# Kernel tuning notes

Hardware: AMD Instinct MI355X
Metric: run time of the kernel (lower is better)

Reference implementation:

```python
import jax, jax.numpy as jnp
import numpy as np

B, S, D, H = 4, 2048, 1024, 16
DEPTH = D // H  # 64


def setup_inputs() -> dict:
    key = jax.random.key(0)
    ks = jax.random.split(key, 11)
    scale = 1.0 / np.sqrt(D)
    inp = {
        "v": jax.random.normal(ks[0], (B, S, D), jnp.float32),
        "k": jax.random.normal(ks[1], (B, S, D), jnp.float32),
        "q": jax.random.normal(ks[2], (B, S, D), jnp.float32),
        # causal mask: 1.0 where attention is disallowed (strict upper triangle)
        "mask": jnp.triu(jnp.ones((S, S), jnp.float32), k=1)[None, None, :, :],
        "wq": jax.random.normal(ks[3], (D, D), jnp.float32) * scale,
        "bq": jnp.zeros((D,), jnp.float32),
        "wk": jax.random.normal(ks[4], (D, D), jnp.float32) * scale,
        "bk": jnp.zeros((D,), jnp.float32),
        "wv": jax.random.normal(ks[5], (D, D), jnp.float32) * scale,
        "bv": jnp.zeros((D,), jnp.float32),
        "wo": jax.random.normal(ks[6], (D, D), jnp.float32) * scale,
        "bo": jnp.zeros((D,), jnp.float32),
    }
    return inp


def _split_heads(x):
    # [B, S, D] -> [B, H, S, depth]
    b, s, _ = x.shape
    return x.reshape(b, s, H, DEPTH).transpose(0, 2, 1, 3)


def reference(v, k, q, mask, wq, bq, wk, bk, wv, bv, wo, bo):
    qh = _split_heads(q @ wq + bq)  # [B,H,S,depth]
    kh = _split_heads(k @ wk + bk)
    vh = _split_heads(v @ wv + bv)

    logits = jnp.einsum("bhqd,bhkd->bhqk", qh, kh) / jnp.sqrt(
        jnp.asarray(DEPTH, jnp.float32)
    )
    logits = logits + mask * -1e9
    attn = jax.nn.softmax(logits, axis=-1)  # [B,H,S,S]
    out = jnp.einsum("bhqk,bhkd->bhqd", attn, vh)
    out = out.transpose(0, 2, 1, 3).reshape(q.shape[0], -1, D)  # [B,S,D]
    return out @ wo + bo
```

## Files before the change

kernel.cpp:

```cpp
#include <hip/hip_runtime.h>

typedef _Float16 f16;
typedef _Float16 half8 __attribute__((ext_vector_type(8)));
typedef _Float16 half4v __attribute__((ext_vector_type(4)));
typedef _Float16 half2v __attribute__((ext_vector_type(2)));
typedef float f32x4 __attribute__((ext_vector_type(4)));

__device__ __forceinline__ void gl_lds16(const void* g, void* l) {
    __builtin_amdgcn_global_load_lds((const __attribute__((address_space(1))) void*)g,
                                     (__attribute__((address_space(3))) void*)l, 16, 0, 0);
}

__device__ __forceinline__ unsigned pack_f16(float a, float b) {
    union { half2v h; unsigned u; } un;
    un.h[0] = (f16)a; un.h[1] = (f16)b;
    return un.u;
}

__device__ __forceinline__ void prep_w_body(const float* __restrict__ W, f16* __restrict__ Wt)
{
    __shared__ float t[64][65];
    const int tid = threadIdx.x;
    const int tk = blockIdx.x * 64, tn = blockIdx.y * 64;
    const int rr = tid >> 4, cc = (tid & 15) * 4;
    #pragma unroll
    for (int j = 0; j < 4; ++j) {
        float4 v = *(const float4*)(W + (size_t)(tk + rr + j * 16) * 1024 + tn + cc);
        t[rr + j * 16][cc] = v.x; t[rr + j * 16][cc + 1] = v.y;
        t[rr + j * 16][cc + 2] = v.z; t[rr + j * 16][cc + 3] = v.w;
    }
    __syncthreads();
    const int n = tid >> 2, kc = (tid & 3) * 16;
    f16 o[16];
    #pragma unroll
    for (int j = 0; j < 16; ++j) o[j] = (f16)t[kc + j][n];
    f16* dst = Wt + (size_t)(tn + n) * 1024 + tk + kc;
    *(uint4*)dst = *(uint4*)o;
    *(uint4*)(dst + 8) = *(uint4*)(o + 8);
}

__global__ __launch_bounds__(256) void prep_w1(const float* __restrict__ W, f16* __restrict__ Wt)
{ prep_w_body(W, Wt); }

__global__ __launch_bounds__(256) void prep_w3(const float* __restrict__ w0,
    const float* __restrict__ w1, const float* __restrict__ w2, f16* __restrict__ Wt)
{
    const int z = blockIdx.z;
    const float* W = (z == 0) ? w0 : (z == 1) ? w1 : w2;
    prep_w_body(W, Wt + (size_t)z * 1024 * 1024);
}

__global__ __launch_bounds__(256, 2) void qkv_gemm(
    const float* __restrict__ Xq, const float* __restrict__ Xk, const float* __restrict__ Xv,
    const f16* __restrict__ Wt,
    const float* __restrict__ bqp, const float* __restrict__ bkp, const float* __restrict__ bvp,
    f16* __restrict__ qh, f16* __restrict__ kh, f16* __restrict__ vth)
{
    __shared__ __align__(16) f16 As[2][128 * 64];
    __shared__ __align__(16) f16 Ws[2][128 * 64];

    const int z = blockIdx.z;
    const float* X    = (z == 0) ? Xq : (z == 1) ? Xk : Xv;
    const float* bias = (z == 0) ? bqp : (z == 1) ? bkp : bvp;
    const f16*   W    = Wt + (size_t)z * 1024 * 1024;

    const int tid = threadIdx.x;
    const int lane = tid & 63;
    const int lane16 = lane & 15, quad = lane >> 4;
    const int wave = tid >> 6;
    const int wm = (wave >> 1) * 64, wn = (wave & 1) * 64;

    const int lin = blockIdx.x + 8 * blockIdx.y;
    const int xcd = lin & 7, t = lin >> 3;
    const int m0 = ((t >> 3) * 8 + xcd) * 128;
    const int n0 = (t & 7) * 128;

    const int wbase = tid & 192;
    const int srow = tid >> 3;
    const int sch  = tid & 7;
    const int swc  = sch ^ (srow & 7);

    const size_t xgbase = (size_t)(m0 + srow) * 1024 + sch * 8;
    const size_t wgbase = (size_t)(n0 + srow) * 1024 + swc * 8;
    f16* const pA0 = As[0] + srow * 64 + swc * 8;
    f16* const pA1 = As[1] + srow * 64 + swc * 8;

    f32x4 acc[4][4] = {};

    {
        float4 xr[4][2];
        #pragma unroll
        for (int i = 0; i < 4; ++i) {
            xr[i][0] = *(const float4*)(X + xgbase + (size_t)i * 32768);
            xr[i][1] = *(const float4*)(X + xgbase + (size_t)i * 32768 + 4);
        }
        #pragma unroll
        for (int i = 0; i < 4; ++i)
            gl_lds16(W + wgbase + (size_t)i * 32768, Ws[0] + (size_t)(i * 256 + wbase) * 8);
        asm volatile("s_waitcnt vmcnt(4)" ::: "memory");
        #pragma unroll
        for (int i = 0; i < 4; ++i) {
            half8 hx;
            hx[0] = (f16)xr[i][0].x; hx[1] = (f16)xr[i][0].y;
            hx[2] = (f16)xr[i][0].z; hx[3] = (f16)xr[i][0].w;
            hx[4] = (f16)xr[i][1].x; hx[5] = (f16)xr[i][1].y;
            hx[6] = (f16)xr[i][1].z; hx[7] = (f16)xr[i][1].w;
            *(half8*)(pA0 + i * 2048) = hx;
        }
        asm volatile("s_waitcnt vmcnt(0) lgkmcnt(0)" ::: "memory");
        __builtin_amdgcn_s_barrier();
        asm volatile("" ::: "memory");
    }

    for (int kt = 0; kt < 16; ++kt) {
        const int cur = kt & 1, nb = cur ^ 1;
        float4 xr[4][2];
        if (kt + 1 < 16) {
            const int k1 = (kt + 1) * 64;
            const float* xs = X + xgbase + k1;
            #pragma unroll
            for (int i = 0; i < 4; ++i) {
                xr[i][0] = *(const float4*)(xs + (size_t)i * 32768);
                xr[i][1] = *(const float4*)(xs + (size_t)i * 32768 + 4);
            }
            const f16* ws = W + wgbase + k1;
            #pragma unroll
            for (int i = 0; i < 4; ++i)
                gl_lds16(ws + (size_t)i * 32768, Ws[nb] + (size_t)(i * 256 + wbase) * 8);
        }

        const f16* Ab = As[cur];
        const f16* Bb = Ws[cur];
        half8 af[4][2], bf[4][2];
        #pragma unroll
        for (int i = 0; i < 4; ++i) {
            const int ra = wm + i * 16 + lane16;
            const int rb = wn + i * 16 + lane16;
            #pragma unroll
            for (int c = 0; c < 2; ++c) {
                af[i][c] = *(const half8*)(Ab + ra * 64 + (((c * 4 + quad) ^ (ra & 7)) * 8));
                bf[i][c] = *(const half8*)(Bb + rb * 64 + (((c * 4 + quad) ^ (rb & 7)) * 8));
            }
        }
        #pragma unroll
        for (int c = 0; c < 2; ++c)
            #pragma unroll
            for (int mi = 0; mi < 4; ++mi)
                #pragma unroll
                for (int ni = 0; ni < 4; ++ni)
                    acc[mi][ni] = __builtin_amdgcn_mfma_f32_16x16x32_f16(af[mi][c], bf[ni][c], acc[mi][ni], 0, 0, 0);

        if (kt + 1 < 16) {
            asm volatile("s_waitcnt vmcnt(4)" ::: "memory");
            f16* pA = (nb == 0) ? pA0 : pA1;
            #pragma unroll
            for (int i = 0; i < 4; ++i) {
                half8 hx;
                hx[0] = (f16)xr[i][0].x; hx[1] = (f16)xr[i][0].y;
                hx[2] = (f16)xr[i][0].z; hx[3] = (f16)xr[i][0].w;
                hx[4] = (f16)xr[i][1].x; hx[5] = (f16)xr[i][1].y;
                hx[6] = (f16)xr[i][1].z; hx[7] = (f16)xr[i][1].w;
                *(half8*)(pA + i * 2048) = hx;
            }
        }
        asm volatile("s_waitcnt vmcnt(0) lgkmcnt(0)" ::: "memory");
        __builtin_amdgcn_s_barrier();
        asm volatile("" ::: "memory");
    }

    #pragma unroll
    for (int mi = 0; mi < 4; ++mi) {
        #pragma unroll
        for (int ni = 0; ni < 4; ++ni) {
            const int col = n0 + wn + ni * 16 + lane16;
            const float bval = bias[col];
            const int grow0 = m0 + wm + mi * 16 + quad * 4;
            if (z == 2) {
                const int b = grow0 >> 11, s0 = grow0 & 2047;
                const int h = col >> 6, d = col & 63;
                half4v p;
                #pragma unroll
                for (int r = 0; r < 4; ++r) p[r] = (f16)(acc[mi][ni][r] + bval);
                *(half4v*)(vth + (((size_t)b * 16 + h) * 64 + d) * 2048 + s0) = p;
            } else {
                f16* out = (z == 0) ? qh : kh;
                #pragma unroll
                for (int r = 0; r < 4; ++r)
                    out[(size_t)(grow0 + r) * 1024 + col] = (f16)(acc[mi][ni][r] + bval);
            }
        }
    }
}

__global__ __launch_bounds__(256, 2) void out_gemm(
    const f16* __restrict__ X, const f16* __restrict__ Wt,
    const float* __restrict__ bias, float* __restrict__ out)
{
    __shared__ __align__(16) f16 As[2][128 * 64];
    __shared__ __align__(16) f16 Bs[2][128 * 64];

    const int tid = threadIdx.x;
    const int lane = tid & 63;
    const int lane16 = lane & 15, quad = lane >> 4;
    const int wave = tid >> 6;
    const int wm = (wave >> 1) * 64, wn = (wave & 1) * 64;

    const int lin = blockIdx.x + 8 * blockIdx.y;
    const int xcd = lin & 7, t = lin >> 3;
    const int m0 = ((t >> 3) * 8 + xcd) * 128;
    const int n0 = (t & 7) * 128;

    const int wbase = tid & 192;
    const int srow = tid >> 3, schunk = tid & 7;
    const int swc = schunk ^ (srow & 7);

    f32x4 acc[4][4] = {};

    #pragma unroll
    for (int i = 0; i < 4; ++i) {
        gl_lds16(Wt + (size_t)(n0 + i * 32 + srow) * 1024 + swc * 8, Bs[0] + (size_t)(i * 256 + wbase) * 8);
        gl_lds16(X  + (size_t)(m0 + i * 32 + srow) * 1024 + swc * 8, As[0] + (size_t)(i * 256 + wbase) * 8);
    }

    for (int kt = 0; kt < 16; ++kt) {
        if (kt + 1 < 16) {
            const int nb = (kt + 1) & 1;
            const int k1 = (kt + 1) * 64;
            #pragma unroll
            for (int i = 0; i < 4; ++i) {
                gl_lds16(Wt + (size_t)(n0 + i * 32 + srow) * 1024 + k1 + swc * 8, Bs[nb] + (size_t)(i * 256 + wbase) * 8);
                gl_lds16(X  + (size_t)(m0 + i * 32 + srow) * 1024 + k1 + swc * 8, As[nb] + (size_t)(i * 256 + wbase) * 8);
            }
            asm volatile("s_waitcnt vmcnt(8)" ::: "memory");
        } else {
            asm volatile("s_waitcnt vmcnt(0)" ::: "memory");
        }
        __builtin_amdgcn_s_barrier();
        asm volatile("" ::: "memory");

        const f16* Ab = As[kt & 1];
        const f16* Bb = Bs[kt & 1];
        half8 af[4][2], bf[4][2];
        #pragma unroll
        for (int i = 0; i < 4; ++i) {
            const int ra = wm + i * 16 + lane16;
            const int rb = wn + i * 16 + lane16;
            #pragma unroll
            for (int c = 0; c < 2; ++c) {
                af[i][c] = *(const half8*)(Ab + ra * 64 + (((c * 4 + quad) ^ (ra & 7)) * 8));
                bf[i][c] = *(const half8*)(Bb + rb * 64 + (((c * 4 + quad) ^ (rb & 7)) * 8));
            }
        }
        #pragma unroll
        for (int c = 0; c < 2; ++c)
            #pragma unroll
            for (int mi = 0; mi < 4; ++mi)
                #pragma unroll
                for (int ni = 0; ni < 4; ++ni)
                    acc[mi][ni] = __builtin_amdgcn_mfma_f32_16x16x32_f16(af[mi][c], bf[ni][c], acc[mi][ni], 0, 0, 0);

        asm volatile("" ::: "memory");
        __builtin_amdgcn_s_barrier();
        asm volatile("" ::: "memory");
    }

    #pragma unroll
    for (int mi = 0; mi < 4; ++mi) {
        #pragma unroll
        for (int ni = 0; ni < 4; ++ni) {
            const int col = n0 + wn + ni * 16 + lane16;
            const float bval = bias[col];
            const int grow0 = m0 + wm + mi * 16 + quad * 4;
            #pragma unroll
            for (int r = 0; r < 4; ++r)
                out[(size_t)(grow0 + r) * 1024 + col] = acc[mi][ni][r] + bval;
        }
    }
}

__global__ __launch_bounds__(256, 4) void attn_kernel(
    const f16* __restrict__ qh, const f16* __restrict__ kh,
    const f16* __restrict__ vt, f16* __restrict__ at)
{
    __shared__ __align__(16) f16 Ks[2][64 * 64];
    __shared__ __align__(16) f16 Vts[2][64 * 64];

    const int tid = threadIdx.x;
    const int lane = tid & 63, wave = tid >> 6;
    const int lane16 = lane & 15, quad = lane >> 4;
    const int wbase = tid & 192;
    const int l3 = lane16 & 7;
    const int srow = tid >> 3, schunk = tid & 7;

    const int lin = blockIdx.x + 16 * blockIdx.y;
    const int xcd = lin & 7, t = lin >> 3;
    const int bh = xcd + 8 * (t & 7);
    const int qi = 15 - (t >> 3);
    const int b = bh >> 4, h = bh & 15;

    const f16* qp = qh + (size_t)b * 2048 * 1024 + h * 64;
    const f16* kp = kh + (size_t)b * 2048 * 1024 + h * 64;
    const f16* vtp = vt + (size_t)bh * 64 * 2048;

    const int qb = 128 * qi;
    const int qrow0 = qb + wave * 32;
    const int ntiles = qb / 64 + 2;
    const int qmax = qrow0 + 31;

    #pragma unroll
    for (int i = 0; i < 2; ++i) {
        const int row = i * 32 + srow;
        const int sw = (schunk ^ (row & 7)) * 8;
        gl_lds16(kp + (size_t)row * 1024 + sw, Ks[0] + (size_t)(i * 256 + wbase) * 8);
        gl_lds16(vtp + (size_t)row * 2048 + sw, Vts[0] + (size_t)(i * 256 + wbase) * 8);
    }

    half8 aq[2][2];
    #pragma unroll
    for (int mt = 0; mt < 2; ++mt)
        #pragma unroll
        for (int c = 0; c < 2; ++c)
            aq[mt][c] = *(const half8*)(qp + (size_t)(qrow0 + mt * 16 + lane16) * 1024 + c * 32 + quad * 8);

    f32x4 o[4][2] = {};
    float lp[2] = {0.0f, 0.0f};

    for (int kt = 0; kt < ntiles; ++kt) {
        if (kt + 1 < ntiles) {
            const int nb = (kt + 1) & 1;
            const int k1 = (kt + 1) * 64;
            #pragma unroll
            for (int i = 0; i < 2; ++i) {
                const int row = i * 32 + srow;
                const int sw = (schunk ^ (row & 7)) * 8;
                gl_lds16(kp + (size_t)(k1 + row) * 1024 + sw, Ks[nb] + (size_t)(i * 256 + wbase) * 8);
                gl_lds16(vtp + (size_t)row * 2048 + k1 + sw, Vts[nb] + (size_t)(i * 256 + wbase) * 8);
            }
            asm volatile("s_waitcnt vmcnt(4)" ::: "memory");
        } else {
            asm volatile("s_waitcnt vmcnt(0)" ::: "memory");
        }
        __builtin_amdgcn_s_barrier();
        asm volatile("" ::: "memory");

        const int k0 = kt * 64;
        if (k0 <= qmax) {
            const f16* Kb = Ks[kt & 1];
            const f16* Vb = Vts[kt & 1];
            f32x4 sT[4][2];
            #pragma unroll
            for (int sub = 0; sub < 4; ++sub) {
                const int kr = sub * 16 + lane16;
                const half8 ak0 = *(const half8*)(Kb + kr * 64 + ((quad ^ l3) * 8));
                const half8 ak1 = *(const half8*)(Kb + kr * 64 + (((4 + quad) ^ l3) * 8));
                #pragma unroll
                for (int mt = 0; mt < 2; ++mt) {
                    f32x4 z = {};
                    z = __builtin_amdgcn_mfma_f32_16x16x32_f16(ak0, aq[mt][0], z, 0, 0, 0);
                    z = __builtin_amdgcn_mfma_f32_16x16x32_f16(ak1, aq[mt][1], z, 0, 0, 0);
                    sT[sub][mt] = z;
                }
            }
            const bool needmask = (k0 + 63 > qrow0);
            if (needmask) {
                #pragma unroll
                for (int sub = 0; sub < 4; ++sub)
                    #pragma unroll
                    for (int mt = 0; mt < 2; ++mt)
                        #pragma unroll
                        for (int r = 0; r < 4; ++r) {
                            const int key = k0 + sub * 16 + quad * 4 + r;
                            const int qi2 = qrow0 + mt * 16 + lane16;
                            if (key > qi2) sT[sub][mt][r] = -1e30f;
                        }
            }

            half8 bp[2][2];
            #pragma unroll
            for (int mt = 0; mt < 2; ++mt) {
                unsigned pk01[4], pk23[4];
                #pragma unroll
                for (int sub = 0; sub < 4; ++sub) {
                    float p[4];
                    #pragma unroll
                    for (int r = 0; r < 4; ++r) {
                        const float x = fmaf(sT[sub][mt][r], 0.18033688011112042f, -5.770780163555852f);
                        float e;
                        asm("v_exp_f32 %0, %1" : "=v"(e) : "v"(x));
                        p[r] = e;
                        lp[mt] += e;
                    }
                    pk01[sub] = pack_f16(p[0], p[1]);
                    pk23[sub] = pack_f16(p[2], p[3]);
                }
                #pragma unroll
                for (int c = 0; c < 2; ++c) {
                    unsigned a0 = pk01[2 * c], b0 = pk01[2 * c + 1];
                    unsigned a1 = pk23[2 * c], b1 = pk23[2 * c + 1];
                    asm("v_permlane32_swap_b32 %0, %1" : "+v"(a0), "+v"(b0));
                    asm("v_permlane16_swap_b32 %0, %1" : "+v"(a0), "+v"(b0));
                    asm("v_permlane32_swap_b32 %0, %1" : "+v"(a1), "+v"(b1));
                    asm("v_permlane16_swap_b32 %0, %1" : "+v"(a1), "+v"(b1));
                    union { unsigned u[4]; half8 h8; } un;
                    un.u[0] = a0; un.u[1] = a1; un.u[2] = b0; un.u[3] = b1;
                    bp[c][mt] = un.h8;
                }
            }

            #pragma unroll
            for (int nt = 0; nt < 4; ++nt) {
                const int dr = nt * 16 + lane16;
                const half8 av0 = *(const half8*)(Vb + dr * 64 + ((quad ^ l3) * 8));
                const half8 av1 = *(const half8*)(Vb + dr * 64 + (((4 + quad) ^ l3) * 8));
                #pragma unroll
                for (int mt = 0; mt < 2; ++mt) {
                    o[nt][mt] = __builtin_amdgcn_mfma_f32_16x16x32_f16(av0, bp[0][mt], o[nt][mt], 0, 0, 0);
                    o[nt][mt] = __builtin_amdgcn_mfma_f32_16x16x32_f16(av1, bp[1][mt], o[nt][mt], 0, 0, 0);
                }
            }
        }
        asm volatile("" ::: "memory");
        __builtin_amdgcn_s_barrier();
        asm volatile("" ::: "memory");
    }

    #pragma unroll
    for (int mt = 0; mt < 2; ++mt) {
        float red = lp[mt];
        red += __shfl_xor(red, 16);
        red += __shfl_xor(red, 32);
        const float inv = 1.0f / red;
        const int sr = qrow0 + mt * 16 + lane16;
        f16* dst = at + ((size_t)b * 2048 + sr) * 1024 + h * 64 + quad * 4;
        #pragma unroll
        for (int nt = 0; nt < 4; ++nt) {
            half4v p;
            #pragma unroll
            for (int r = 0; r < 4; ++r) p[r] = (f16)(o[nt][mt][r] * inv);
            *(half4v*)(dst + nt * 16) = p;
        }
    }
}

extern "C" void kernel_launch(void* const* d_in, const int* in_sizes, int n_in,
                              void* d_out, int out_size, void* d_ws, size_t ws_size,
                              hipStream_t stream)
{
    const float* v  = (const float*)d_in[0];
    const float* k  = (const float*)d_in[1];
    const float* q  = (const float*)d_in[2];
    const float* wq = (const float*)d_in[4];
    const float* bq = (const float*)d_in[5];
    const float* wk = (const float*)d_in[6];
    const float* bk = (const float*)d_in[7];
    const float* wv = (const float*)d_in[8];
    const float* bv = (const float*)d_in[9];
    const float* wo = (const float*)d_in[10];
    const float* bo = (const float*)d_in[11];

    f16* qh = (f16*)d_ws;
    f16* kh = qh + (size_t)8 * 1024 * 1024;
    f16* vt = kh + (size_t)8 * 1024 * 1024;
    f16* at = vt + (size_t)8 * 1024 * 1024;

    f16* wT = (f16*)d_out;
    f16* woT = qh;

    prep_w3<<<dim3(16, 16, 3), 256, 0, stream>>>(wq, wk, wv, wT);

    qkv_gemm<<<dim3(8, 64, 3), 256, 0, stream>>>(q, k, v, wT, bq, bk, bv, qh, kh, vt);

    attn_kernel<<<dim3(16, 64), 256, 0, stream>>>(qh, kh, vt, at);

    prep_w1<<<dim3(16, 16), 256, 0, stream>>>(wo, woT);
    out_gemm<<<dim3(8, 64), 256, 0, stream>>>(at, woT, bo, (float*)d_out);
}
```

Baseline: 330.7 us.

## Enlarge QKV GEMM tile to 256x256 with 8 waves and split-phase pipelining

The QKV projection GEMM moves from 128x128 tiles with 4 waves to 256x256 tiles with 8 waves, each wave computing a 128x64 sub-tile. Each k-step is split into two MFMA halves with a barrier between them, and the W prefetch plus the X convert-and-store into LDS are interleaved with the second half. s_setprio is raised around the MFMA blocks. The aim is more data reuse per LDS byte and better overlap of loads with compute, at the cost of doubled LDS use (128KB), more accumulator registers, and fewer blocks (384), which may limit occupancy and load balance.

```diff
diff --git a/kernel.cpp b/kernel.cpp
--- a/kernel.cpp
+++ b/kernel.cpp
@@ -50,14 +50,14 @@
     prep_w_body(W, Wt + (size_t)z * 1024 * 1024);
 }
 
-__global__ __launch_bounds__(256, 2) void qkv_gemm(
+__global__ __launch_bounds__(512, 2) void qkv_gemm(
     const float* __restrict__ Xq, const float* __restrict__ Xk, const float* __restrict__ Xv,
     const f16* __restrict__ Wt,
     const float* __restrict__ bqp, const float* __restrict__ bkp, const float* __restrict__ bvp,
     f16* __restrict__ qh, f16* __restrict__ kh, f16* __restrict__ vth)
 {
-    __shared__ __align__(16) f16 As[2][128 * 64];
-    __shared__ __align__(16) f16 Ws[2][128 * 64];
+    __shared__ __align__(16) f16 As[2][256 * 64];
+    __shared__ __align__(16) f16 Bs[2][256 * 64];
 
     const int z = blockIdx.z;
     const float* X    = (z == 0) ? Xq : (z == 1) ? Xk : Xv;
@@ -68,35 +68,34 @@
     const int lane = tid & 63;
     const int lane16 = lane & 15, quad = lane >> 4;
     const int wave = tid >> 6;
-    const int wm = (wave >> 1) * 64, wn = (wave & 1) * 64;
-
-    const int lin = blockIdx.x + 8 * blockIdx.y;
+    const int wm = (wave & 1) * 128;
+    const int wn = (wave >> 1) * 64;
+
+    const int lin = blockIdx.x + 4 * blockIdx.y;
     const int xcd = lin & 7, t = lin >> 3;
-    const int m0 = ((t >> 3) * 8 + xcd) * 128;
-    const int n0 = (t & 7) * 128;
-
-    const int wbase = tid & 192;
+    const int m0 = (((t >> 2) << 3) | xcd) * 256;
+    const int n0 = (t & 3) * 256;
+
     const int srow = tid >> 3;
     const int sch  = tid & 7;
     const int swc  = sch ^ (srow & 7);
 
     const size_t xgbase = (size_t)(m0 + srow) * 1024 + sch * 8;
     const size_t wgbase = (size_t)(n0 + srow) * 1024 + swc * 8;
-    f16* const pA0 = As[0] + srow * 64 + swc * 8;
-    f16* const pA1 = As[1] + srow * 64 + swc * 8;
-
-    f32x4 acc[4][4] = {};
+    const int wldsbase = (tid & 448) * 8;
+
+    f32x4 acc[8][4] = {};
 
     {
         float4 xr[4][2];
         #pragma unroll
         for (int i = 0; i < 4; ++i) {
-            xr[i][0] = *(const float4*)(X + xgbase + (size_t)i * 32768);
-            xr[i][1] = *(const float4*)(X + xgbase + (size_t)i * 32768 + 4);
+            xr[i][0] = *(const float4*)(X + xgbase + (size_t)i * 65536);
+            xr[i][1] = *(const float4*)(X + xgbase + (size_t)i * 65536 + 4);
         }
         #pragma unroll
         for (int i = 0; i < 4; ++i)
-            gl_lds16(W + wgbase + (size_t)i * 32768, Ws[0] + (size_t)(i * 256 + wbase) * 8);
+            gl_lds16(W + wgbase + (size_t)i * 65536, Bs[0] + i * 4096 + wldsbase);
         asm volatile("s_waitcnt vmcnt(4)" ::: "memory");
         #pragma unroll
         for (int i = 0; i < 4; ++i) {
@@ -105,7 +104,7 @@
             hx[2] = (f16)xr[i][0].z; hx[3] = (f16)xr[i][0].w;
             hx[4] = (f16)xr[i][1].x; hx[5] = (f16)xr[i][1].y;
             hx[6] = (f16)xr[i][1].z; hx[7] = (f16)xr[i][1].w;
-            *(half8*)(pA0 + i * 2048) = hx;
+            *(half8*)(As[0] + i * 4096 + srow * 64 + swc * 8) = hx;
         }
         asm volatile("s_waitcnt vmcnt(0) lgkmcnt(0)" ::: "memory");
         __builtin_amdgcn_s_barrier();
@@ -114,45 +113,58 @@
 
     for (int kt = 0; kt < 16; ++kt) {
         const int cur = kt & 1, nb = cur ^ 1;
+        const bool pf = (kt + 1 < 16);
+        const f16* Ab = As[cur];
+        const f16* Bb = Bs[cur];
+
         float4 xr[4][2];
-        if (kt + 1 < 16) {
-            const int k1 = (kt + 1) * 64;
-            const float* xs = X + xgbase + k1;
+        if (pf) {
+            const float* xs = X + xgbase + (kt + 1) * 64;
             #pragma unroll
             for (int i = 0; i < 4; ++i) {
-                xr[i][0] = *(const float4*)(xs + (size_t)i * 32768);
-                xr[i][1] = *(const float4*)(xs + (size_t)i * 32768 + 4);
-            }
-            const f16* ws = W + wgbase + k1;
-            #pragma unroll
-            for (int i = 0; i < 4; ++i)
-                gl_lds16(ws + (size_t)i * 32768, Ws[nb] + (size_t)(i * 256 + wbase) * 8);
-        }
-
-        const f16* Ab = As[cur];
-        const f16* Bb = Ws[cur];
-        half8 af[4][2], bf[4][2];
+                xr[i][0] = *(const float4*)(xs + (size_t)i * 65536);
+                xr[i][1] = *(const float4*)(xs + (size_t)i * 65536 + 4);
+            }
+        }
+        half8 af0[4][2], bf[4][2];
         #pragma unroll
         for (int i = 0; i < 4; ++i) {
             const int ra = wm + i * 16 + lane16;
             const int rb = wn + i * 16 + lane16;
             #pragma unroll
             for (int c = 0; c < 2; ++c) {
-                af[i][c] = *(const half8*)(Ab + ra * 64 + (((c * 4 + quad) ^ (ra & 7)) * 8));
-                bf[i][c] = *(const half8*)(Bb + rb * 64 + (((c * 4 + quad) ^ (rb & 7)) * 8));
-            }
-        }
+                af0[i][c] = *(const half8*)(Ab + ra * 64 + (((c * 4 + quad) ^ (ra & 7)) * 8));
+                bf[i][c]  = *(const half8*)(Bb + rb * 64 + (((c * 4 + quad) ^ (rb & 7)) * 8));
+            }
+        }
+        asm volatile("s_waitcnt lgkmcnt(0)" ::: "memory");
+        __builtin_amdgcn_s_setprio(1);
         #pragma unroll
         for (int c = 0; c < 2; ++c)
             #pragma unroll
             for (int mi = 0; mi < 4; ++mi)
                 #pragma unroll
                 for (int ni = 0; ni < 4; ++ni)
-                    acc[mi][ni] = __builtin_amdgcn_mfma_f32_16x16x32_f16(af[mi][c], bf[ni][c], acc[mi][ni], 0, 0, 0);
-
-        if (kt + 1 < 16) {
+                    acc[mi][ni] = __builtin_amdgcn_mfma_f32_16x16x32_f16(af0[mi][c], bf[ni][c], acc[mi][ni], 0, 0, 0);
+        __builtin_amdgcn_s_setprio(0);
+        asm volatile("" ::: "memory");
+        __builtin_amdgcn_s_barrier();
+        asm volatile("" ::: "memory");
+
+        half8 af1[4][2];
+        #pragma unroll
+        for (int i = 0; i < 4; ++i) {
+            const int ra = wm + 64 + i * 16 + lane16;
+            #pragma unroll
+            for (int c = 0; c < 2; ++c)
+                af1[i][c] = *(const half8*)(Ab + ra * 64 + (((c * 4 + quad) ^ (ra & 7)) * 8));
+        }
+        if (pf) {
+            const f16* ws = W + wgbase + (kt + 1) * 64;
+            #pragma unroll
+            for (int i = 0; i < 4; ++i)
+                gl_lds16(ws + (size_t)i * 65536, Bs[nb] + i * 4096 + wldsbase);
             asm volatile("s_waitcnt vmcnt(4)" ::: "memory");
-            f16* pA = (nb == 0) ? pA0 : pA1;
             #pragma unroll
             for (int i = 0; i < 4; ++i) {
                 half8 hx;
@@ -160,16 +172,27 @@
                 hx[2] = (f16)xr[i][0].z; hx[3] = (f16)xr[i][0].w;
                 hx[4] = (f16)xr[i][1].x; hx[5] = (f16)xr[i][1].y;
                 hx[6] = (f16)xr[i][1].z; hx[7] = (f16)xr[i][1].w;
-                *(half8*)(pA + i * 2048) = hx;
-            }
-        }
-        asm volatile("s_waitcnt vmcnt(0) lgkmcnt(0)" ::: "memory");
-        __builtin_amdgcn_s_barrier();
-        asm volatile("" ::: "memory");
-    }
-
-    #pragma unroll
-    for (int mi = 0; mi < 4; ++mi) {
+                *(half8*)(As[nb] + i * 4096 + srow * 64 + swc * 8) = hx;
+            }
+        }
+        asm volatile("s_waitcnt lgkmcnt(0)" ::: "memory");
+        __builtin_amdgcn_s_setprio(1);
+        #pragma unroll
+        for (int c = 0; c < 2; ++c)
+            #pragma unroll
+            for (int mi = 0; mi < 4; ++mi)
+                #pragma unroll
+                for (int ni = 0; ni < 4; ++ni)
+                    acc[4 + mi][ni] = __builtin_amdgcn_mfma_f32_16x16x32_f16(af1[mi][c], bf[ni][c], acc[4 + mi][ni], 0, 0, 0);
+        __builtin_amdgcn_s_setprio(0);
+        if (pf) asm volatile("s_waitcnt vmcnt(0)" ::: "memory");
+        asm volatile("" ::: "memory");
+        __builtin_amdgcn_s_barrier();
+        asm volatile("" ::: "memory");
+    }
+
+    #pragma unroll
+    for (int mi = 0; mi < 8; ++mi) {
         #pragma unroll
         for (int ni = 0; ni < 4; ++ni) {
             const int col = n0 + wn + ni * 16 + lane16;
@@ -468,7 +491,7 @@
 
     prep_w3<<<dim3(16, 16, 3), 256, 0, stream>>>(wq, wk, wv, wT);
 
-    qkv_gemm<<<dim3(8, 64, 3), 256, 0, stream>>>(q, k, v, wT, bq, bk, bv, qh, kh, vt);
+    qkv_gemm<<<dim3(4, 32, 3), 512, 0, stream>>>(q, k, v, wT, bq, bk, bv, qh, kh, vt);
 
     attn_kernel<<<dim3(16, 64), 256, 0, stream>>>(qh, kh, vt, at);
 
```

Result: no change. 329.1 us (-0.5%).

## Retile QKV GEMM to 128x256 blocks with 512 threads and K-step 32

Applied to the files above, without the earlier changes.

The QKV projection GEMM now uses 512-thread blocks, each covering a 128x256 output tile, with the K dimension stepped in chunks of 32 instead of 64. The LDS tiles shrink to allow four blocks per CU, and the swizzle is changed to a 4-chunk XOR pattern. Each block reuses its activation tile across twice as many output columns, cutting redundant fp32 X reads. In exchange it needs twice as many loop iterations and barriers, with less MFMA work between each sync.

```diff
diff --git a/kernel.cpp b/kernel.cpp
--- a/kernel.cpp
+++ b/kernel.cpp
@@ -50,14 +50,14 @@
     prep_w_body(W, Wt + (size_t)z * 1024 * 1024);
 }
 
-__global__ __launch_bounds__(256, 2) void qkv_gemm(
+__global__ __launch_bounds__(512, 4) void qkv_gemm(
     const float* __restrict__ Xq, const float* __restrict__ Xk, const float* __restrict__ Xv,
     const f16* __restrict__ Wt,
     const float* __restrict__ bqp, const float* __restrict__ bkp, const float* __restrict__ bvp,
     f16* __restrict__ qh, f16* __restrict__ kh, f16* __restrict__ vth)
 {
-    __shared__ __align__(16) f16 As[2][128 * 64];
-    __shared__ __align__(16) f16 Ws[2][128 * 64];
+    __shared__ __align__(16) f16 As[2][128 * 32];
+    __shared__ __align__(16) f16 Bs[2][256 * 32];
 
     const int z = blockIdx.z;
     const float* X    = (z == 0) ? Xq : (z == 1) ? Xk : Xv;
@@ -67,101 +67,78 @@
     const int tid = threadIdx.x;
     const int lane = tid & 63;
     const int lane16 = lane & 15, quad = lane >> 4;
+    const int l2 = lane16 & 3;
     const int wave = tid >> 6;
-    const int wm = (wave >> 1) * 64, wn = (wave & 1) * 64;
-
-    const int lin = blockIdx.x + 8 * blockIdx.y;
+    const int wm = (wave & 1) * 64;
+    const int wn = (wave >> 1) * 64;
+
+    const int lin = blockIdx.x + 4 * blockIdx.y;
     const int xcd = lin & 7, t = lin >> 3;
-    const int m0 = ((t >> 3) * 8 + xcd) * 128;
-    const int n0 = (t & 7) * 128;
-
-    const int wbase = tid & 192;
-    const int srow = tid >> 3;
-    const int sch  = tid & 7;
-    const int swc  = sch ^ (srow & 7);
-
-    const size_t xgbase = (size_t)(m0 + srow) * 1024 + sch * 8;
-    const size_t wgbase = (size_t)(n0 + srow) * 1024 + swc * 8;
-    f16* const pA0 = As[0] + srow * 64 + swc * 8;
-    f16* const pA1 = As[1] + srow * 64 + swc * 8;
+    const int m0 = (((t >> 2) << 3) | xcd) * 128;
+    const int n0 = (t & 3) * 256;
+
+    const int xrow = tid >> 2, xch = tid & 3;
+    const size_t xgbase = (size_t)(m0 + xrow) * 1024 + xch * 8;
+    f16* const pA0 = As[0] + xrow * 32 + ((xch ^ (xrow & 3)) * 8);
+    f16* const pA1 = As[1] + xrow * 32 + ((xch ^ (xrow & 3)) * 8);
+
+    const int wrow0 = tid >> 2;
+    const int wch = tid & 3;
+    const size_t wg0 = (size_t)(n0 + wrow0) * 1024 + ((wch ^ (wrow0 & 3)) * 8);
+    const size_t wg1 = (size_t)(n0 + 128 + wrow0) * 1024 + ((wch ^ (wrow0 & 3)) * 8);
+    const int wldsbase = (tid & 448) * 8;
 
     f32x4 acc[4][4] = {};
 
     {
-        float4 xr[4][2];
-        #pragma unroll
-        for (int i = 0; i < 4; ++i) {
-            xr[i][0] = *(const float4*)(X + xgbase + (size_t)i * 32768);
-            xr[i][1] = *(const float4*)(X + xgbase + (size_t)i * 32768 + 4);
-        }
+        float4 x0 = *(const float4*)(X + xgbase);
+        float4 x1 = *(const float4*)(X + xgbase + 4);
+        gl_lds16(W + wg0, Bs[0] + wldsbase);
+        gl_lds16(W + wg1, Bs[0] + 4096 + wldsbase);
+        asm volatile("s_waitcnt vmcnt(2)" ::: "memory");
+        half8 hx;
+        hx[0] = (f16)x0.x; hx[1] = (f16)x0.y; hx[2] = (f16)x0.z; hx[3] = (f16)x0.w;
+        hx[4] = (f16)x1.x; hx[5] = (f16)x1.y; hx[6] = (f16)x1.z; hx[7] = (f16)x1.w;
+        *(half8*)pA0 = hx;
+        asm volatile("s_waitcnt vmcnt(0) lgkmcnt(0)" ::: "memory");
+        __builtin_amdgcn_s_barrier();
+        asm volatile("" ::: "memory");
+    }
+
+    for (int kt = 0; kt < 32; ++kt) {
+        const int cur = kt & 1;
+        const bool pf = (kt + 1 < 32);
+        const f16* Ab = As[cur];
+        const f16* Bb = Bs[cur];
+
+        float4 x0, x1;
+        if (pf) {
+            const int k1 = (kt + 1) * 32;
+            x0 = *(const float4*)(X + xgbase + k1);
+            x1 = *(const float4*)(X + xgbase + k1 + 4);
+            gl_lds16(W + wg0 + k1, Bs[cur ^ 1] + wldsbase);
+            gl_lds16(W + wg1 + k1, Bs[cur ^ 1] + 4096 + wldsbase);
+        }
+
+        half8 af[4], bf[4];
         #pragma unroll
         for (int i = 0; i < 4; ++i)
-            gl_lds16(W + wgbase + (size_t)i * 32768, Ws[0] + (size_t)(i * 256 + wbase) * 8);
-        asm volatile("s_waitcnt vmcnt(4)" ::: "memory");
-        #pragma unroll
-        for (int i = 0; i < 4; ++i) {
+            af[i] = *(const half8*)(Ab + (wm + i * 16 + lane16) * 32 + ((quad ^ l2) * 8));
+        #pragma unroll
+        for (int i = 0; i < 4; ++i)
+            bf[i] = *(const half8*)(Bb + (wn + i * 16 + lane16) * 32 + ((quad ^ l2) * 8));
+        #pragma unroll
+        for (int mi = 0; mi < 4; ++mi)
+            #pragma unroll
+            for (int ni = 0; ni < 4; ++ni)
+                acc[mi][ni] = __builtin_amdgcn_mfma_f32_16x16x32_f16(af[mi], bf[ni], acc[mi][ni], 0, 0, 0);
+
+        if (pf) {
+            asm volatile("s_waitcnt vmcnt(2)" ::: "memory");
             half8 hx;
-            hx[0] = (f16)xr[i][0].x; hx[1] = (f16)xr[i][0].y;
-            hx[2] = (f16)xr[i][0].z; hx[3] = (f16)xr[i][0].w;
-            hx[4] = (f16)xr[i][1].x; hx[5] = (f16)xr[i][1].y;
-            hx[6] = (f16)xr[i][1].z; hx[7] = (f16)xr[i][1].w;
-            *(half8*)(pA0 + i * 2048) = hx;
-        }
-        asm volatile("s_waitcnt vmcnt(0) lgkmcnt(0)" ::: "memory");
-        __builtin_amdgcn_s_barrier();
-        asm volatile("" ::: "memory");
-    }
-
-    for (int kt = 0; kt < 16; ++kt) {
-        const int cur = kt & 1, nb = cur ^ 1;
-        float4 xr[4][2];
-        if (kt + 1 < 16) {
-            const int k1 = (kt + 1) * 64;
-            const float* xs = X + xgbase + k1;
-            #pragma unroll
-            for (int i = 0; i < 4; ++i) {
-                xr[i][0] = *(const float4*)(xs + (size_t)i * 32768);
-                xr[i][1] = *(const float4*)(xs + (size_t)i * 32768 + 4);
-            }
-            const f16* ws = W + wgbase + k1;
-            #pragma unroll
-            for (int i = 0; i < 4; ++i)
-                gl_lds16(ws + (size_t)i * 32768, Ws[nb] + (size_t)(i * 256 + wbase) * 8);
-        }
-
-        const f16* Ab = As[cur];
-        const f16* Bb = Ws[cur];
-        half8 af[4][2], bf[4][2];
-        #pragma unroll
-        for (int i = 0; i < 4; ++i) {
-            const int ra = wm + i * 16 + lane16;
-            const int rb = wn + i * 16 + lane16;
-            #pragma unroll
-            for (int c = 0; c < 2; ++c) {
-                af[i][c] = *(const half8*)(Ab + ra * 64 + (((c * 4 + quad) ^ (ra & 7)) * 8));
-                bf[i][c] = *(const half8*)(Bb + rb * 64 + (((c * 4 + quad) ^ (rb & 7)) * 8));
-            }
-        }
-        #pragma unroll
-        for (int c = 0; c < 2; ++c)
-            #pragma unroll
-            for (int mi = 0; mi < 4; ++mi)
-                #pragma unroll
-                for (int ni = 0; ni < 4; ++ni)
-                    acc[mi][ni] = __builtin_amdgcn_mfma_f32_16x16x32_f16(af[mi][c], bf[ni][c], acc[mi][ni], 0, 0, 0);
-
-        if (kt + 1 < 16) {
-            asm volatile("s_waitcnt vmcnt(4)" ::: "memory");
-            f16* pA = (nb == 0) ? pA0 : pA1;
-            #pragma unroll
-            for (int i = 0; i < 4; ++i) {
-                half8 hx;
-                hx[0] = (f16)xr[i][0].x; hx[1] = (f16)xr[i][0].y;
-                hx[2] = (f16)xr[i][0].z; hx[3] = (f16)xr[i][0].w;
-                hx[4] = (f16)xr[i][1].x; hx[5] = (f16)xr[i][1].y;
-                hx[6] = (f16)xr[i][1].z; hx[7] = (f16)xr[i][1].w;
-                *(half8*)(pA + i * 2048) = hx;
-            }
+            hx[0] = (f16)x0.x; hx[1] = (f16)x0.y; hx[2] = (f16)x0.z; hx[3] = (f16)x0.w;
+            hx[4] = (f16)x1.x; hx[5] = (f16)x1.y; hx[6] = (f16)x1.z; hx[7] = (f16)x1.w;
+            *(half8*)((cur == 1) ? pA0 : pA1) = hx;
         }
         asm volatile("s_waitcnt vmcnt(0) lgkmcnt(0)" ::: "memory");
         __builtin_amdgcn_s_barrier();
@@ -468,7 +445,7 @@
 
     prep_w3<<<dim3(16, 16, 3), 256, 0, stream>>>(wq, wk, wv, wT);
 
-    qkv_gemm<<<dim3(8, 64, 3), 256, 0, stream>>>(q, k, v, wT, bq, bk, bv, qh, kh, vt);
+    qkv_gemm<<<dim3(4, 64, 3), 512, 0, stream>>>(q, k, v, wT, bq, bk, bv, qh, kh, vt);
 
     attn_kernel<<<dim3(16, 64), 256, 0, stream>>>(qh, kh, vt, at);
 
```

Result: no change. 324.7 us (-1.8%).
